# Performance work log

Hardware: AMD Instinct MI355X
Metric: run time of the kernel (lower is better)

## Reference

```python
import jax, jax.numpy as jnp
import numpy as np

B, S, D = 2048, 8, 1280
K = 1                 # n_components_remove
HIGH_T = 0.6          # PC1_HIGH_ACTIVITY_THRESHOLD
STORM_T = 0.8         # solar_storm_threshold


def setup_inputs() -> dict:
    key = jax.random.key(0)
    k1, k2 = jax.random.split(key, 2)
    features = jax.random.normal(k1, (B, S, D), dtype=jnp.float32)
    kp_index = jax.random.uniform(k2, (B,), dtype=jnp.float32) * 9.0
    cmr_gate = jnp.ones((1,), dtype=jnp.float32)  # nn.Parameter(torch.ones(1))
    return {"features": features, "kp_index": kp_index, "cmr_gate": cmr_gate}


def reference(features, kp_index, cmr_gate):
    # Per-sample standardization over the feature axis (numpy std, ddof=0)
    mu = features.mean(axis=2, keepdims=True)            # (B, S, 1)
    sigma = features.std(axis=2, keepdims=True) + 1e-8   # (B, S, 1)
    fn = (features - mu) / sigma                         # (B, S, D)

    # Batched thin SVD of the (S, D) normalized feature matrix
    U, sv, Vt = jnp.linalg.svd(fn, full_matrices=False)  # (B,S,S), (B,S), (B,S,D)
    var = sv * sv
    pc1_ratio = var[:, 0] / (var.sum(axis=-1) + 1e-8)    # (B,)

    # solar_flag: 0 normal, 1 high activity, 2 storm
    solar_flag = (pc1_ratio >= HIGH_T).astype(jnp.int32) + (pc1_ratio >= STORM_T).astype(jnp.int32)

    # Rank-K reconstruction of the common-mode (solar) component
    low = jnp.einsum('bsk,bk,bkd->bsd', U[:, :, :K], sv[:, :K], Vt[:, :K, :])
    clean = (fn - low) * sigma + mu                      # de-normalized cleaned features

    # Kp-gating: amplify CMR when Kp >= 5
    kp_gate = 1.0 + 0.5 * (kp_index >= 5.0).astype(features.dtype)[:, None, None]
    clean = features + kp_gate * (clean - features)

    # Learnable gate
    gate = jax.nn.sigmoid(cmr_gate)[0]
    features_clean = features + gate * (clean - features)
    return features_clean, pc1_ratio, solar_flag
```

## Files before the change

kernel.cpp:

```cpp
#include <hip/hip_runtime.h>
#include <math.h>


#define SV 8
#define DV 1280
#define D4 320
#define BSTRIDE (SV*DV)
#define GSZ 136
#define SPLIT 4
#define CITER (40/SPLIT)
#define WSS 17

typedef __attribute__((ext_vector_type(8))) short bf16x8;
typedef __attribute__((ext_vector_type(4))) float f32x4;

union BF8 { bf16x8 v; short s[8]; unsigned u[4]; };

__global__ __launch_bounds__(256)
void cmr_gram(const float* __restrict__ feat, float* __restrict__ gram)
{
    const int lane = threadIdx.x & 63;
    const int wid  = (blockIdx.x * 256 + threadIdx.x) >> 6;
    const int pair = wid >> 2;
    const int h    = wid & (SPLIT - 1);
    const int m    = lane & 15;
    const int quad = lane >> 4;
    const int bt   = m >> 3;
    const int row  = m & 7;

    const float* __restrict__ fb =
        feat + ((size_t)(pair * 2 + bt)) * BSTRIDE + (size_t)row * DV;

    BF8 ones;
#pragma unroll
    for (int j = 0; j < 4; ++j) ones.u[j] = 0x3F803F80u;

    f32x4 accHH = {0.f, 0.f, 0.f, 0.f};
    f32x4 accHL = {0.f, 0.f, 0.f, 0.f};
    f32x4 accS  = {0.f, 0.f, 0.f, 0.f};

#pragma unroll
    for (int c = 0; c < CITER; ++c) {
        const int k0 = (h * CITER + c) * 32 + quad * 8;
        const float4 x0 = *(const float4*)(fb + k0);
        const float4 x1 = *(const float4*)(fb + k0 + 4);
        float x[8] = {x0.x, x0.y, x0.z, x0.w, x1.x, x1.y, x1.z, x1.w};
        BF8 hi, lo;
#pragma unroll
        for (int j = 0; j < 4; ++j) {
            unsigned hp, lp;
            asm("v_cvt_pk_bf16_f32 %0, %1, %2" : "=v"(hp) : "v"(x[2*j]), "v"(x[2*j+1]));
            const float h0 = __uint_as_float(hp << 16);
            const float h1 = __uint_as_float(hp & 0xFFFF0000u);
            const float l0 = x[2*j]     - h0;
            const float l1 = x[2*j + 1] - h1;
            asm("v_cvt_pk_bf16_f32 %0, %1, %2" : "=v"(lp) : "v"(l0), "v"(l1));
            hi.u[j] = hp;
            lo.u[j] = lp;
        }
        accHH = __builtin_amdgcn_mfma_f32_16x16x32_bf16(hi.v, hi.v,   accHH, 0, 0, 0);
        accHL = __builtin_amdgcn_mfma_f32_16x16x32_bf16(hi.v, lo.v,   accHL, 0, 0, 0);
        accS  = __builtin_amdgcn_mfma_f32_16x16x32_bf16(hi.v, ones.v, accS,  0, 0, 0);
        accS  = __builtin_amdgcn_mfma_f32_16x16x32_bf16(lo.v, ones.v, accS,  0, 0, 0);
    }

    const int colb = (lane & 15) >> 3;
    const int col  = lane & 7;
#pragma unroll
    for (int r = 0; r < 4; ++r) {
        const int rowg = quad * 4 + r;
        if ((rowg >> 3) == colb) {
            float* gb = gram + ((size_t)((pair * 2 + colb) * SPLIT + h)) * GSZ;
            gb[(rowg & 7) * 8 + col]      = accHH[r];
            gb[64 + (rowg & 7) * 8 + col] = accHL[r];
        }
    }
    if ((lane & 15) == 0) {
#pragma unroll
        for (int r = 0; r < 4; ++r) {
            const int rowg = quad * 4 + r;
            gram[((size_t)((pair * 2 + (rowg >> 3)) * SPLIT + h)) * GSZ
                 + 128 + (rowg & 7)] = accS[r];
        }
    }
}

__global__ __launch_bounds__(64, 1)
void cmr_eigen(const float* __restrict__ gram,
               const float* __restrict__ kp,
               const float* __restrict__ cmr_gate,
               float* __restrict__ coef,
               float* __restrict__ out,
               int Bn)
{
    const int b = blockIdx.x * 64 + threadIdx.x;
    const float* __restrict__ g = gram + (size_t)b * (GSZ * SPLIT);

    float G[8][8], S[8], mu[8], sig[8], rsig[8];
#pragma unroll
    for (int i = 0; i < 8; ++i) {
#pragma unroll
        for (int j = 0; j < 8; ++j) G[i][j] = 0.f;
        S[i] = 0.f;
    }
#pragma unroll
    for (int hh = 0; hh < SPLIT; ++hh) {
        const float* __restrict__ gh = g + hh * GSZ;
#pragma unroll
        for (int i = 0; i < 8; ++i) {
#pragma unroll
            for (int j = 0; j < 8; ++j)
                G[i][j] += gh[i * 8 + j] + gh[64 + i * 8 + j] + gh[64 + j * 8 + i];
            S[i] += gh[128 + i];
        }
    }
    const float invD = 1.f / (float)DV;
#pragma unroll
    for (int i = 0; i < 8; ++i) {
        mu[i] = S[i] * invD;
        const float var = fmaxf(G[i][i] * invD - mu[i] * mu[i], 0.f);
        sig[i]  = sqrtf(var) + 1e-8f;
        rsig[i] = 1.f / sig[i];
    }
#pragma unroll
    for (int i = 0; i < 8; ++i)
#pragma unroll
        for (int j = 0; j < 8; ++j)
            G[i][j] = (G[i][j] - (float)DV * mu[i] * mu[j]) * rsig[i] * rsig[j];

    float tr = 0.f;
#pragma unroll
    for (int i = 0; i < 8; ++i) tr += G[i][i];

    float A[8][8];
    {
        const float rt = 1.f / fmaxf(tr, 1e-30f);
#pragma unroll
        for (int i = 0; i < 8; ++i)
#pragma unroll
            for (int j = 0; j < 8; ++j) A[i][j] = G[i][j] * rt;
    }
#pragma unroll
    for (int t = 0; t < 12; ++t) {
        float Bm[8][8];
        float trB = 0.f;
#pragma unroll
        for (int i = 0; i < 8; ++i)
#pragma unroll
            for (int j = i; j < 8; ++j) {
                float acc = 0.f;
#pragma unroll
                for (int k = 0; k < 8; ++k)
                    acc = fmaf(A[i][k], A[j][k], acc);
                Bm[i][j] = acc;
                if (i == j) trB += acc;
            }
        const float rt = 1.f / fmaxf(trB, 1e-30f);
#pragma unroll
        for (int i = 0; i < 8; ++i)
#pragma unroll
            for (int j = i; j < 8; ++j) {
                const float v = Bm[i][j] * rt;
                A[i][j] = v; A[j][i] = v;
            }
    }
    int bj = 0; float best = A[0][0];
#pragma unroll
    for (int k = 1; k < 8; ++k)
        if (A[k][k] > best) { best = A[k][k]; bj = k; }
    float u[8];
#pragma unroll
    for (int i = 0; i < 8; ++i) {
        float v = A[i][0];
#pragma unroll
        for (int k = 1; k < 8; ++k) v = (bj == k) ? A[i][k] : v;
        u[i] = v;
    }
    {
        float nn = 0.f;
#pragma unroll
        for (int i = 0; i < 8; ++i) nn = fmaf(u[i], u[i], nn);
        const float r = rsqrtf(fmaxf(nn, 1e-30f));
#pragma unroll
        for (int i = 0; i < 8; ++i) u[i] *= r;
    }
#pragma unroll
    for (int it = 0; it < 2; ++it) {
        float y[8]; float ny = 0.f;
#pragma unroll
        for (int i = 0; i < 8; ++i) {
            float acc = 0.f;
#pragma unroll
            for (int k = 0; k < 8; ++k) acc = fmaf(G[i][k], u[k], acc);
            y[i] = acc; ny = fmaf(acc, acc, ny);
        }
        const float r = rsqrtf(fmaxf(ny, 1e-30f));
#pragma unroll
        for (int i = 0; i < 8; ++i) u[i] = y[i] * r;
    }
    float lam = 0.f;
#pragma unroll
    for (int i = 0; i < 8; ++i) {
        float acc = 0.f;
#pragma unroll
        for (int k = 0; k < 8; ++k) acc = fmaf(G[i][k], u[k], acc);
        lam = fmaf(u[i], acc, lam);
    }
    const float pc1 = lam / (tr + 1e-8f);

    const float gate = 1.f / (1.f + expf(-cmr_gate[0]));
    const float kpg  = (kp[b] >= 5.0f) ? 1.5f : 1.0f;
    const float Gt   = gate * kpg;

    float bc = 0.f;
#pragma unroll
    for (int i = 0; i < 8; ++i) bc = fmaf(u[i] * rsig[i], mu[i], bc);

    float* wsb = coef + (size_t)b * WSS;
#pragma unroll
    for (int i = 0; i < 8; ++i) {
        wsb[i]     = u[i] * rsig[i];
        wsb[8 + i] = Gt * sig[i] * u[i];
    }
    wsb[16] = bc;
    out[(size_t)Bn * BSTRIDE + b] = pc1;
    out[(size_t)Bn * BSTRIDE + Bn + b] =
        (pc1 >= 0.6f ? 1.f : 0.f) + (pc1 >= 0.8f ? 1.f : 0.f);
}

__global__ __launch_bounds__(320)
void cmr_apply(const float* __restrict__ feat,
               const float* __restrict__ coef,
               float* __restrict__ out)
{
    const int tid  = threadIdx.x;
    const int lane = tid & 63;
    const int wq   = tid >> 6;
    const int b    = blockIdx.x;

    const float* __restrict__ wsb = coef + (size_t)b * WSS;
    float a[8], c[8];
#pragma unroll
    for (int s = 0; s < 8; ++s) { a[s] = wsb[s]; c[s] = wsb[8 + s]; }
    const float bc = wsb[16];

    const float4* __restrict__ f4 = (const float4*)(feat + (size_t)b * BSTRIDE);
    float4* __restrict__ o4 = (float4*)(out + (size_t)b * BSTRIDE);
    const int d4 = wq * 64 + lane;

    float4 f[8];
#pragma unroll
    for (int s = 0; s < 8; ++s) f[s] = f4[s * D4 + d4];

    float4 p = make_float4(-bc, -bc, -bc, -bc);
#pragma unroll
    for (int s = 0; s < 8; ++s) {
        p.x = fmaf(a[s], f[s].x, p.x);
        p.y = fmaf(a[s], f[s].y, p.y);
        p.z = fmaf(a[s], f[s].z, p.z);
        p.w = fmaf(a[s], f[s].w, p.w);
    }
#pragma unroll
    for (int s = 0; s < 8; ++s) {
        float4 o;
        o.x = fmaf(-c[s], p.x, f[s].x);
        o.y = fmaf(-c[s], p.y, f[s].y);
        o.z = fmaf(-c[s], p.z, f[s].z);
        o.w = fmaf(-c[s], p.w, f[s].w);
        o4[s * D4 + d4] = o;
    }
}

extern "C" void kernel_launch(void* const* d_in, const int* in_sizes, int n_in,
                              void* d_out, int out_size, void* d_ws, size_t ws_size,
                              hipStream_t stream) {
    const float* feat = (const float*)d_in[0];
    const float* kp   = (const float*)d_in[1];
    const float* gate = (const float*)d_in[2];
    float* out = (float*)d_out;
    const int Bn = in_sizes[0] / BSTRIDE;

    float* gram = (float*)d_ws;
    float* coef = gram + (size_t)Bn * GSZ * SPLIT;

    cmr_gram <<<(Bn / 8) * SPLIT, 256, 0, stream>>>(feat, gram);
    cmr_eigen<<<Bn / 64, 64,  0, stream>>>(gram, kp, gate, coef, out, Bn);
    cmr_apply<<<Bn,      320, 0, stream>>>(feat, coef, out);
}
```

Measured before the change: 181.7 us.

## Fuse gram, eigen and apply kernels into one per-pair block kernel

```diff
diff --git a/kernel.cpp b/kernel.cpp
--- a/kernel.cpp
+++ b/kernel.cpp
@@ -9,265 +9,261 @@
 #define GSZ 136
 #define SPLIT 4
 #define CITER (40/SPLIT)
-#define WSS 17
 
 typedef __attribute__((ext_vector_type(8))) short bf16x8;
 typedef __attribute__((ext_vector_type(4))) float f32x4;
 
 union BF8 { bf16x8 v; short s[8]; unsigned u[4]; };
 
-__global__ __launch_bounds__(256)
-void cmr_gram(const float* __restrict__ feat, float* __restrict__ gram)
+__global__ __launch_bounds__(256, 2)
+void cmr_fused(const float* __restrict__ feat,
+               const float* __restrict__ kp,
+               const float* __restrict__ cmr_gate,
+               float* __restrict__ out, int Bn)
 {
-    const int lane = threadIdx.x & 63;
-    const int wid  = (blockIdx.x * 256 + threadIdx.x) >> 6;
-    const int pair = wid >> 2;
-    const int h    = wid & (SPLIT - 1);
-    const int m    = lane & 15;
-    const int quad = lane >> 4;
-    const int bt   = m >> 3;
-    const int row  = m & 7;
-
-    const float* __restrict__ fb =
-        feat + ((size_t)(pair * 2 + bt)) * BSTRIDE + (size_t)row * DV;
-
-    BF8 ones;
-#pragma unroll
-    for (int j = 0; j < 4; ++j) ones.u[j] = 0x3F803F80u;
-
-    f32x4 accHH = {0.f, 0.f, 0.f, 0.f};
-    f32x4 accHL = {0.f, 0.f, 0.f, 0.f};
-    f32x4 accS  = {0.f, 0.f, 0.f, 0.f};
-
-#pragma unroll
-    for (int c = 0; c < CITER; ++c) {
-        const int k0 = (h * CITER + c) * 32 + quad * 8;
-        const float4 x0 = *(const float4*)(fb + k0);
-        const float4 x1 = *(const float4*)(fb + k0 + 4);
-        float x[8] = {x0.x, x0.y, x0.z, x0.w, x1.x, x1.y, x1.z, x1.w};
-        BF8 hi, lo;
-#pragma unroll
-        for (int j = 0; j < 4; ++j) {
-            unsigned hp, lp;
-            asm("v_cvt_pk_bf16_f32 %0, %1, %2" : "=v"(hp) : "v"(x[2*j]), "v"(x[2*j+1]));
-            const float h0 = __uint_as_float(hp << 16);
-            const float h1 = __uint_as_float(hp & 0xFFFF0000u);
-            const float l0 = x[2*j]     - h0;
-            const float l1 = x[2*j + 1] - h1;
-            asm("v_cvt_pk_bf16_f32 %0, %1, %2" : "=v"(lp) : "v"(l0), "v"(l1));
-            hi.u[j] = hp;
-            lo.u[j] = lp;
-        }
-        accHH = __builtin_amdgcn_mfma_f32_16x16x32_bf16(hi.v, hi.v,   accHH, 0, 0, 0);
-        accHL = __builtin_amdgcn_mfma_f32_16x16x32_bf16(hi.v, lo.v,   accHL, 0, 0, 0);
-        accS  = __builtin_amdgcn_mfma_f32_16x16x32_bf16(hi.v, ones.v, accS,  0, 0, 0);
-        accS  = __builtin_amdgcn_mfma_f32_16x16x32_bf16(lo.v, ones.v, accS,  0, 0, 0);
-    }
-
-    const int colb = (lane & 15) >> 3;
-    const int col  = lane & 7;
-#pragma unroll
-    for (int r = 0; r < 4; ++r) {
-        const int rowg = quad * 4 + r;
-        if ((rowg >> 3) == colb) {
-            float* gb = gram + ((size_t)((pair * 2 + colb) * SPLIT + h)) * GSZ;
-            gb[(rowg & 7) * 8 + col]      = accHH[r];
-            gb[64 + (rowg & 7) * 8 + col] = accHL[r];
-        }
-    }
-    if ((lane & 15) == 0) {
+    __shared__ float lg[SPLIT][2][GSZ];
+    __shared__ float lc[2][17];
+
+    const int tid  = threadIdx.x;
+    const int lane = tid & 63;
+    const int h    = tid >> 6;
+    const int pair = blockIdx.x;
+
+    {
+        const int m    = lane & 15;
+        const int quad = lane >> 4;
+        const int bt   = m >> 3;
+        const int row  = m & 7;
+
+        const float* __restrict__ fb =
+            feat + ((size_t)(pair * 2 + bt)) * BSTRIDE + (size_t)row * DV;
+
+        BF8 ones;
+#pragma unroll
+        for (int j = 0; j < 4; ++j) ones.u[j] = 0x3F803F80u;
+
+        f32x4 accHH = {0.f, 0.f, 0.f, 0.f};
+        f32x4 accHL = {0.f, 0.f, 0.f, 0.f};
+        f32x4 accS  = {0.f, 0.f, 0.f, 0.f};
+
+#pragma unroll
+        for (int c = 0; c < CITER; ++c) {
+            const int k0 = (h * CITER + c) * 32 + quad * 8;
+            const float4 x0 = *(const float4*)(fb + k0);
+            const float4 x1 = *(const float4*)(fb + k0 + 4);
+            float x[8] = {x0.x, x0.y, x0.z, x0.w, x1.x, x1.y, x1.z, x1.w};
+            BF8 hi, lo;
+#pragma unroll
+            for (int j = 0; j < 4; ++j) {
+                unsigned hp, lp;
+                asm("v_cvt_pk_bf16_f32 %0, %1, %2"
+                    : "=v"(hp) : "v"(x[2*j]), "v"(x[2*j+1]));
+                const float h0 = __uint_as_float(hp << 16);
+                const float h1 = __uint_as_float(hp & 0xFFFF0000u);
+                const float l0 = x[2*j]     - h0;
+                const float l1 = x[2*j + 1] - h1;
+                asm("v_cvt_pk_bf16_f32 %0, %1, %2"
+                    : "=v"(lp) : "v"(l0), "v"(l1));
+                hi.u[j] = hp;
+                lo.u[j] = lp;
+            }
+            accHH = __builtin_amdgcn_mfma_f32_16x16x32_bf16(hi.v, hi.v,   accHH, 0, 0, 0);
+            accHL = __builtin_amdgcn_mfma_f32_16x16x32_bf16(hi.v, lo.v,   accHL, 0, 0, 0);
+            accS  = __builtin_amdgcn_mfma_f32_16x16x32_bf16(hi.v, ones.v, accS,  0, 0, 0);
+            accS  = __builtin_amdgcn_mfma_f32_16x16x32_bf16(lo.v, ones.v, accS,  0, 0, 0);
+        }
+
+        const int colb = (lane & 15) >> 3;
+        const int col  = lane & 7;
 #pragma unroll
         for (int r = 0; r < 4; ++r) {
             const int rowg = quad * 4 + r;
-            gram[((size_t)((pair * 2 + (rowg >> 3)) * SPLIT + h)) * GSZ
-                 + 128 + (rowg & 7)] = accS[r];
+            if ((rowg >> 3) == colb) {
+                lg[h][colb][(rowg & 7) * 8 + col]      = accHH[r];
+                lg[h][colb][64 + (rowg & 7) * 8 + col] = accHL[r];
+            }
+        }
+        if ((lane & 15) == 0) {
+#pragma unroll
+            for (int r = 0; r < 4; ++r) {
+                const int rowg = quad * 4 + r;
+                lg[h][rowg >> 3][128 + (rowg & 7)] = accS[r];
+            }
         }
     }
-}
-
-__global__ __launch_bounds__(64, 1)
-void cmr_eigen(const float* __restrict__ gram,
-               const float* __restrict__ kp,
-               const float* __restrict__ cmr_gate,
-               float* __restrict__ coef,
-               float* __restrict__ out,
-               int Bn)
-{
-    const int b = blockIdx.x * 64 + threadIdx.x;
-    const float* __restrict__ g = gram + (size_t)b * (GSZ * SPLIT);
-
-    float G[8][8], S[8], mu[8], sig[8], rsig[8];
-#pragma unroll
-    for (int i = 0; i < 8; ++i) {
-#pragma unroll
-        for (int j = 0; j < 8; ++j) G[i][j] = 0.f;
-        S[i] = 0.f;
+    __syncthreads();
+
+    if (h == 0 && lane < 2) {
+        const int b2 = lane;
+        const int b  = pair * 2 + b2;
+
+        float G[8][8], S[8], mu[8], sig[8], rsig[8];
+#pragma unroll
+        for (int i = 0; i < 8; ++i) {
+#pragma unroll
+            for (int j = 0; j < 8; ++j) G[i][j] = 0.f;
+            S[i] = 0.f;
+        }
+#pragma unroll
+        for (int hh = 0; hh < SPLIT; ++hh) {
+            const float* __restrict__ gh = &lg[hh][b2][0];
+#pragma unroll
+            for (int i = 0; i < 8; ++i) {
+#pragma unroll
+                for (int j = 0; j < 8; ++j)
+                    G[i][j] += gh[i * 8 + j] + gh[64 + i * 8 + j] + gh[64 + j * 8 + i];
+                S[i] += gh[128 + i];
+            }
+        }
+        const float invD = 1.f / (float)DV;
+#pragma unroll
+        for (int i = 0; i < 8; ++i) {
+            mu[i] = S[i] * invD;
+            const float var = fmaxf(G[i][i] * invD - mu[i] * mu[i], 0.f);
+            sig[i]  = sqrtf(var) + 1e-8f;
+            rsig[i] = 1.f / sig[i];
+        }
+#pragma unroll
+        for (int i = 0; i < 8; ++i)
+#pragma unroll
+            for (int j = 0; j < 8; ++j)
+                G[i][j] = (G[i][j] - (float)DV * mu[i] * mu[j]) * rsig[i] * rsig[j];
+
+        float tr = 0.f;
+#pragma unroll
+        for (int i = 0; i < 8; ++i) tr += G[i][i];
+
+        float A[8][8];
+        {
+            const float rt = 1.f / fmaxf(tr, 1e-30f);
+#pragma unroll
+            for (int i = 0; i < 8; ++i)
+#pragma unroll
+                for (int j = 0; j < 8; ++j) A[i][j] = G[i][j] * rt;
+        }
+#pragma unroll
+        for (int t = 0; t < 12; ++t) {
+            float Bm[8][8];
+            float trB = 0.f;
+#pragma unroll
+            for (int i = 0; i < 8; ++i)
+#pragma unroll
+                for (int j = i; j < 8; ++j) {
+                    float acc = 0.f;
+#pragma unroll
+                    for (int k = 0; k < 8; ++k)
+                        acc = fmaf(A[i][k], A[j][k], acc);
+                    Bm[i][j] = acc;
+                    if (i == j) trB += acc;
+                }
+            const float rt = 1.f / fmaxf(trB, 1e-30f);
+#pragma unroll
+            for (int i = 0; i < 8; ++i)
+#pragma unroll
+                for (int j = i; j < 8; ++j) {
+                    const float v = Bm[i][j] * rt;
+                    A[i][j] = v; A[j][i] = v;
+                }
+        }
+        int bj = 0; float best = A[0][0];
+#pragma unroll
+        for (int k = 1; k < 8; ++k)
+            if (A[k][k] > best) { best = A[k][k]; bj = k; }
+        float u[8];
+#pragma unroll
+        for (int i = 0; i < 8; ++i) {
+            float v = A[i][0];
+#pragma unroll
+            for (int k = 1; k < 8; ++k) v = (bj == k) ? A[i][k] : v;
+            u[i] = v;
+        }
+        {
+            float nn = 0.f;
+#pragma unroll
+            for (int i = 0; i < 8; ++i) nn = fmaf(u[i], u[i], nn);
+            const float r = rsqrtf(fmaxf(nn, 1e-30f));
+#pragma unroll
+            for (int i = 0; i < 8; ++i) u[i] *= r;
+        }
+#pragma unroll
+        for (int it = 0; it < 2; ++it) {
+            float y[8]; float ny = 0.f;
+#pragma unroll
+            for (int i = 0; i < 8; ++i) {
+                float acc = 0.f;
+#pragma unroll
+                for (int k = 0; k < 8; ++k) acc = fmaf(G[i][k], u[k], acc);
+                y[i] = acc; ny = fmaf(acc, acc, ny);
+            }
+            const float r = rsqrtf(fmaxf(ny, 1e-30f));
+#pragma unroll
+            for (int i = 0; i < 8; ++i) u[i] = y[i] * r;
+        }
+        float lam = 0.f;
+#pragma unroll
+        for (int i = 0; i < 8; ++i) {
+            float acc = 0.f;
+#pragma unroll
+            for (int k = 0; k < 8; ++k) acc = fmaf(G[i][k], u[k], acc);
+            lam = fmaf(u[i], acc, lam);
+        }
+        const float pc1 = lam / (tr + 1e-8f);
+
+        const float gate = 1.f / (1.f + expf(-cmr_gate[0]));
+        const float kpg  = (kp[b] >= 5.0f) ? 1.5f : 1.0f;
+        const float Gt   = gate * kpg;
+
+        float bc = 0.f;
+#pragma unroll
+        for (int i = 0; i < 8; ++i) bc = fmaf(u[i] * rsig[i], mu[i], bc);
+
+#pragma unroll
+        for (int i = 0; i < 8; ++i) {
+            lc[b2][i]     = u[i] * rsig[i];
+            lc[b2][8 + i] = Gt * sig[i] * u[i];
+        }
+        lc[b2][16] = bc;
+        out[(size_t)Bn * BSTRIDE + b] = pc1;
+        out[(size_t)Bn * BSTRIDE + Bn + b] =
+            (pc1 >= 0.6f ? 1.f : 0.f) + (pc1 >= 0.8f ? 1.f : 0.f);
     }
-#pragma unroll
-    for (int hh = 0; hh < SPLIT; ++hh) {
-        const float* __restrict__ gh = g + hh * GSZ;
-#pragma unroll
-        for (int i = 0; i < 8; ++i) {
-#pragma unroll
-            for (int j = 0; j < 8; ++j)
-                G[i][j] += gh[i * 8 + j] + gh[64 + i * 8 + j] + gh[64 + j * 8 + i];
-            S[i] += gh[128 + i];
-        }
-    }
-    const float invD = 1.f / (float)DV;
-#pragma unroll
-    for (int i = 0; i < 8; ++i) {
-        mu[i] = S[i] * invD;
-        const float var = fmaxf(G[i][i] * invD - mu[i] * mu[i], 0.f);
-        sig[i]  = sqrtf(var) + 1e-8f;
-        rsig[i] = 1.f / sig[i];
-    }
-#pragma unroll
-    for (int i = 0; i < 8; ++i)
-#pragma unroll
-        for (int j = 0; j < 8; ++j)
-            G[i][j] = (G[i][j] - (float)DV * mu[i] * mu[j]) * rsig[i] * rsig[j];
-
-    float tr = 0.f;
-#pragma unroll
-    for (int i = 0; i < 8; ++i) tr += G[i][i];
-
-    float A[8][8];
-    {
-        const float rt = 1.f / fmaxf(tr, 1e-30f);
-#pragma unroll
-        for (int i = 0; i < 8; ++i)
-#pragma unroll
-            for (int j = 0; j < 8; ++j) A[i][j] = G[i][j] * rt;
-    }
-#pragma unroll
-    for (int t = 0; t < 12; ++t) {
-        float Bm[8][8];
-        float trB = 0.f;
-#pragma unroll
-        for (int i = 0; i < 8; ++i)
-#pragma unroll
-            for (int j = i; j < 8; ++j) {
-                float acc = 0.f;
-#pragma unroll
-                for (int k = 0; k < 8; ++k)
-                    acc = fmaf(A[i][k], A[j][k], acc);
-                Bm[i][j] = acc;
-                if (i == j) trB += acc;
-            }
-        const float rt = 1.f / fmaxf(trB, 1e-30f);
-#pragma unroll
-        for (int i = 0; i < 8; ++i)
-#pragma unroll
-            for (int j = i; j < 8; ++j) {
-                const float v = Bm[i][j] * rt;
-                A[i][j] = v; A[j][i] = v;
-            }
-    }
-    int bj = 0; float best = A[0][0];
-#pragma unroll
-    for (int k = 1; k < 8; ++k)
-        if (A[k][k] > best) { best = A[k][k]; bj = k; }
-    float u[8];
-#pragma unroll
-    for (int i = 0; i < 8; ++i) {
-        float v = A[i][0];
-#pragma unroll
-        for (int k = 1; k < 8; ++k) v = (bj == k) ? A[i][k] : v;
-        u[i] = v;
-    }
-    {
-        float nn = 0.f;
-#pragma unroll
-        for (int i = 0; i < 8; ++i) nn = fmaf(u[i], u[i], nn);
-        const float r = rsqrtf(fmaxf(nn, 1e-30f));
-#pragma unroll
-        for (int i = 0; i < 8; ++i) u[i] *= r;
-    }
-#pragma unroll
-    for (int it = 0; it < 2; ++it) {
-        float y[8]; float ny = 0.f;
-#pragma unroll
-        for (int i = 0; i < 8; ++i) {
-            float acc = 0.f;
-#pragma unroll
-            for (int k = 0; k < 8; ++k) acc = fmaf(G[i][k], u[k], acc);
-            y[i] = acc; ny = fmaf(acc, acc, ny);
-        }
-        const float r = rsqrtf(fmaxf(ny, 1e-30f));
-#pragma unroll
-        for (int i = 0; i < 8; ++i) u[i] = y[i] * r;
-    }
-    float lam = 0.f;
-#pragma unroll
-    for (int i = 0; i < 8; ++i) {
-        float acc = 0.f;
-#pragma unroll
-        for (int k = 0; k < 8; ++k) acc = fmaf(G[i][k], u[k], acc);
-        lam = fmaf(u[i], acc, lam);
-    }
-    const float pc1 = lam / (tr + 1e-8f);
-
-    const float gate = 1.f / (1.f + expf(-cmr_gate[0]));
-    const float kpg  = (kp[b] >= 5.0f) ? 1.5f : 1.0f;
-    const float Gt   = gate * kpg;
-
-    float bc = 0.f;
-#pragma unroll
-    for (int i = 0; i < 8; ++i) bc = fmaf(u[i] * rsig[i], mu[i], bc);
-
-    float* wsb = coef + (size_t)b * WSS;
-#pragma unroll
-    for (int i = 0; i < 8; ++i) {
-        wsb[i]     = u[i] * rsig[i];
-        wsb[8 + i] = Gt * sig[i] * u[i];
-    }
-    wsb[16] = bc;
-    out[(size_t)Bn * BSTRIDE + b] = pc1;
-    out[(size_t)Bn * BSTRIDE + Bn + b] =
-        (pc1 >= 0.6f ? 1.f : 0.f) + (pc1 >= 0.8f ? 1.f : 0.f);
-}
-
-__global__ __launch_bounds__(320)
-void cmr_apply(const float* __restrict__ feat,
-               const float* __restrict__ coef,
-               float* __restrict__ out)
-{
-    const int tid  = threadIdx.x;
-    const int lane = tid & 63;
-    const int wq   = tid >> 6;
-    const int b    = blockIdx.x;
-
-    const float* __restrict__ wsb = coef + (size_t)b * WSS;
-    float a[8], c[8];
-#pragma unroll
-    for (int s = 0; s < 8; ++s) { a[s] = wsb[s]; c[s] = wsb[8 + s]; }
-    const float bc = wsb[16];
-
-    const float4* __restrict__ f4 = (const float4*)(feat + (size_t)b * BSTRIDE);
-    float4* __restrict__ o4 = (float4*)(out + (size_t)b * BSTRIDE);
-    const int d4 = wq * 64 + lane;
-
-    float4 f[8];
-#pragma unroll
-    for (int s = 0; s < 8; ++s) f[s] = f4[s * D4 + d4];
-
-    float4 p = make_float4(-bc, -bc, -bc, -bc);
-#pragma unroll
-    for (int s = 0; s < 8; ++s) {
-        p.x = fmaf(a[s], f[s].x, p.x);
-        p.y = fmaf(a[s], f[s].y, p.y);
-        p.z = fmaf(a[s], f[s].z, p.z);
-        p.w = fmaf(a[s], f[s].w, p.w);
-    }
-#pragma unroll
-    for (int s = 0; s < 8; ++s) {
-        float4 o;
-        o.x = fmaf(-c[s], p.x, f[s].x);
-        o.y = fmaf(-c[s], p.y, f[s].y);
-        o.z = fmaf(-c[s], p.z, f[s].z);
-        o.w = fmaf(-c[s], p.w, f[s].w);
-        o4[s * D4 + d4] = o;
+    __syncthreads();
+
+    for (int u = tid; u < 2 * D4; u += 256) {
+        const int b2  = (u >= D4) ? 1 : 0;
+        const int col = u - b2 * D4;
+
+        float a[8], c[8];
+#pragma unroll
+        for (int s = 0; s < 8; ++s) { a[s] = lc[b2][s]; c[s] = lc[b2][8 + s]; }
+        const float bc = lc[b2][16];
+
+        const float4* __restrict__ f4 =
+            (const float4*)(feat + (size_t)(pair * 2 + b2) * BSTRIDE);
+        float4* __restrict__ o4 =
+            (float4*)(out + (size_t)(pair * 2 + b2) * BSTRIDE);
+
+        float4 f[8];
+#pragma unroll
+        for (int s = 0; s < 8; ++s) f[s] = f4[s * D4 + col];
+
+        float4 p = make_float4(-bc, -bc, -bc, -bc);
+#pragma unroll
+        for (int s = 0; s < 8; ++s) {
+            p.x = fmaf(a[s], f[s].x, p.x);
+            p.y = fmaf(a[s], f[s].y, p.y);
+            p.z = fmaf(a[s], f[s].z, p.z);
+            p.w = fmaf(a[s], f[s].w, p.w);
+        }
+#pragma unroll
+        for (int s = 0; s < 8; ++s) {
+            float4 o;
+            o.x = fmaf(-c[s], p.x, f[s].x);
+            o.y = fmaf(-c[s], p.y, f[s].y);
+            o.z = fmaf(-c[s], p.z, f[s].z);
+            o.w = fmaf(-c[s], p.w, f[s].w);
+            o4[s * D4 + col] = o;
+        }
     }
 }
 
@@ -279,11 +275,7 @@
     const float* gate = (const float*)d_in[2];
     float* out = (float*)d_out;
     const int Bn = in_sizes[0] / BSTRIDE;
-
-    float* gram = (float*)d_ws;
-    float* coef = gram + (size_t)Bn * GSZ * SPLIT;
-
-    cmr_gram <<<(Bn / 8) * SPLIT, 256, 0, stream>>>(feat, gram);
-    cmr_eigen<<<Bn / 64, 64,  0, stream>>>(gram, kp, gate, coef, out, Bn);
-    cmr_apply<<<Bn,      320, 0, stream>>>(feat, coef, out);
+    (void)d_ws; (void)ws_size;
+
+    cmr_fused<<<Bn / 2, 256, 0, stream>>>(feat, kp, gate, out, Bn);
 }
```

New measurement: 178.0 us. 2.1% less time.
